# Optimization experiments

Measured on AMD Instinct MI355X. Metric: run time of the kernel, lower is better.

## Reference

```python
import jax, jax.numpy as jnp
import numpy as np

N_NODES = 100000
D_FEAT = 256
BATCH = 16384
K_SAMPLE = 10


def setup_inputs() -> dict:
    key = jax.random.key(0)
    k1, k2, k3, k4 = jax.random.split(key, 4)
    features = jax.random.normal(k1, (N_NODES, D_FEAT), dtype=jnp.float32)
    neigh_idx = jax.random.randint(k2, (BATCH, K_SAMPLE), 0, N_NODES, dtype=jnp.int64)
    nodes = jax.random.randint(k3, (BATCH,), 0, N_NODES, dtype=jnp.int64)
    # models np.random.permutation row shuffle of the embedding matrix
    perm = jax.random.permutation(k4, N_NODES).astype(jnp.int64)
    return {"features": features, "neigh_idx": neigh_idx, "nodes": nodes, "perm": perm}


def reference(features, neigh_idx, nodes, perm):
    # mask.mm(embed): mean over K sampled neighbors' features  -> [B, D]
    to_feats = jnp.mean(features[neigh_idx], axis=1)
    # shuffled embedding matrix = features[perm]; mask.mm(shuf_embed)
    shuf_to_feats = jnp.mean(features[perm[neigh_idx]], axis=1)
    # mask_self.mm(embed): gather own-node row  -> [B, D]
    skip_feats = features[nodes]
    shuf_skip_feats = features[perm[nodes]]
    return (to_feats, shuf_to_feats, skip_feats, shuf_skip_feats)
```

## Files before the change

### kernel.cpp

```cpp
#include <hip/hip_runtime.h>


typedef float f32x4 __attribute__((ext_vector_type(4)));

constexpr int BATCH    = 16384;
constexpr int K_SAMPLE = 10;
constexpr int D_FEAT   = 256;
constexpr int SLICES   = 8;
constexpr int SLICE_D  = D_FEAT / SLICES;
constexpr int CHUNK    = 32;
constexpr int THREADS  = 256;

__global__ __launch_bounds__(THREADS)
void mean_agg_kernel(const float* __restrict__ features,
                     const int*   __restrict__ neigh_idx,
                     const int*   __restrict__ nodes,
                     const int*   __restrict__ perm,
                     float*       __restrict__ out)
{
    const int slice = blockIdx.x & (SLICES - 1);
    const int chunk = blockIdx.x >> 3;

    const int t     = threadIdx.x;
    const int g     = t >> 3;
    const int lane8 = t & 7;

    const int b = chunk * CHUNK + g;
    const int d = slice * SLICE_D + lane8 * 4;

    const int n  = nodes[b];
    const int pn = perm[n];
    const f32x4 o2 = *reinterpret_cast<const f32x4*>(
        &features[(size_t)n  * D_FEAT + d]);
    const f32x4 o3 = *reinterpret_cast<const f32x4*>(
        &features[(size_t)pn * D_FEAT + d]);

    f32x4 acc  = {0.f, 0.f, 0.f, 0.f};
    f32x4 accs = {0.f, 0.f, 0.f, 0.f};

    #pragma unroll
    for (int k = 0; k < K_SAMPLE; ++k) {
        const int idx  = neigh_idx[b * K_SAMPLE + k];
        const int pidx = perm[idx];
        const f32x4 f  = *reinterpret_cast<const f32x4*>(
            &features[(size_t)idx  * D_FEAT + d]);
        const f32x4 fs = *reinterpret_cast<const f32x4*>(
            &features[(size_t)pidx * D_FEAT + d]);
        acc  += f;
        accs += fs;
    }

    const float inv = 1.0f / (float)K_SAMPLE;
    const f32x4 o0 = acc  * inv;
    const f32x4 o1 = accs * inv;

    const size_t row = (size_t)b * D_FEAT + d;
    const size_t sec = (size_t)BATCH * D_FEAT;
    __builtin_nontemporal_store(o0, reinterpret_cast<f32x4*>(&out[row]          ));
    __builtin_nontemporal_store(o1, reinterpret_cast<f32x4*>(&out[row +     sec]));
    __builtin_nontemporal_store(o2, reinterpret_cast<f32x4*>(&out[row + 2 * sec]));
    __builtin_nontemporal_store(o3, reinterpret_cast<f32x4*>(&out[row + 3 * sec]));
}

extern "C" void kernel_launch(void* const* d_in, const int* in_sizes, int n_in,
                              void* d_out, int out_size, void* d_ws, size_t ws_size,
                              hipStream_t stream) {
    const float* features  = (const float*)d_in[0];
    const int*   neigh_idx = (const int*)  d_in[1];
    const int*   nodes     = (const int*)  d_in[2];
    const int*   perm      = (const int*)  d_in[3];
    float*       out       = (float*)d_out;

    const int grid = (BATCH / CHUNK) * SLICES;
    mean_agg_kernel<<<grid, THREADS, 0, stream>>>(features, neigh_idx, nodes, perm, out);
}
```

Baseline: 59.61 us.

## Stage gather indices in LDS and split feature gathers into node-range phases

Loads neighbor indices, node ids and their perm lookups once per block into shared memory instead of redundantly per lane group. Splits the feature gather loop into four phases by node-index range, separated by block barriers, aiming to improve cache locality of the random row reads. The phasing adds branches and barriers that limit how many independent loads are in flight, and the locality benefit depends on blocks progressing in step, which is not enforced across the grid.

```diff
diff --git a/kernel.cpp b/kernel.cpp
--- a/kernel.cpp
+++ b/kernel.cpp
@@ -6,10 +6,13 @@
 constexpr int BATCH    = 16384;
 constexpr int K_SAMPLE = 10;
 constexpr int D_FEAT   = 256;
+constexpr int N_NODES  = 100000;
 constexpr int SLICES   = 8;
 constexpr int SLICE_D  = D_FEAT / SLICES;
 constexpr int CHUNK    = 32;
 constexpr int THREADS  = 256;
+constexpr int PHASES   = 4;
+constexpr int RANGE    = N_NODES / PHASES;
 
 __global__ __launch_bounds__(THREADS)
 void mean_agg_kernel(const float* __restrict__ features,
@@ -28,26 +31,53 @@
     const int b = chunk * CHUNK + g;
     const int d = slice * SLICE_D + lane8 * 4;
 
-    const int n  = nodes[b];
-    const int pn = perm[n];
-    const f32x4 o2 = *reinterpret_cast<const f32x4*>(
-        &features[(size_t)n  * D_FEAT + d]);
-    const f32x4 o3 = *reinterpret_cast<const f32x4*>(
-        &features[(size_t)pn * D_FEAT + d]);
+    __shared__ int s_idx [CHUNK * K_SAMPLE];
+    __shared__ int s_pidx[CHUNK * K_SAMPLE];
+    __shared__ int s_n [CHUNK];
+    __shared__ int s_pn[CHUNK];
+
+    for (int i = t; i < CHUNK * K_SAMPLE; i += THREADS) {
+        const int idx = neigh_idx[chunk * CHUNK * K_SAMPLE + i];
+        s_idx [i] = idx;
+        s_pidx[i] = perm[idx];
+    }
+    if (t < CHUNK) {
+        const int n = nodes[chunk * CHUNK + t];
+        s_n [t] = n;
+        s_pn[t] = perm[n];
+    }
+    __syncthreads();
 
     f32x4 acc  = {0.f, 0.f, 0.f, 0.f};
     f32x4 accs = {0.f, 0.f, 0.f, 0.f};
+    f32x4 o2   = {0.f, 0.f, 0.f, 0.f};
+    f32x4 o3   = {0.f, 0.f, 0.f, 0.f};
 
-    #pragma unroll
-    for (int k = 0; k < K_SAMPLE; ++k) {
-        const int idx  = neigh_idx[b * K_SAMPLE + k];
-        const int pidx = perm[idx];
-        const f32x4 f  = *reinterpret_cast<const f32x4*>(
-            &features[(size_t)idx  * D_FEAT + d]);
-        const f32x4 fs = *reinterpret_cast<const f32x4*>(
-            &features[(size_t)pidx * D_FEAT + d]);
-        acc  += f;
-        accs += fs;
+    for (int p = 0; p < PHASES; ++p) {
+        const int lo = p * RANGE;
+        const int hi = lo + RANGE;
+
+        #pragma unroll
+        for (int k = 0; k < K_SAMPLE; ++k) {
+            const int idx = s_idx[g * K_SAMPLE + k];
+            if (idx >= lo && idx < hi)
+                acc += *reinterpret_cast<const f32x4*>(
+                    &features[(size_t)idx * D_FEAT + d]);
+            const int pidx = s_pidx[g * K_SAMPLE + k];
+            if (pidx >= lo && pidx < hi)
+                accs += *reinterpret_cast<const f32x4*>(
+                    &features[(size_t)pidx * D_FEAT + d]);
+        }
+        const int n = s_n[g];
+        if (n >= lo && n < hi)
+            o2 = *reinterpret_cast<const f32x4*>(
+                &features[(size_t)n * D_FEAT + d]);
+        const int pn = s_pn[g];
+        if (pn >= lo && pn < hi)
+            o3 = *reinterpret_cast<const f32x4*>(
+                &features[(size_t)pn * D_FEAT + d]);
+
+        __syncthreads();
     }
 
     const float inv = 1.0f / (float)K_SAMPLE;
```

Result: slower. 74.26 us (+24.6%).

## Split neighbor gathers into node-range phases to improve cache locality

Applied to the files above, without the earlier changes.

Preloads all neighbor and permuted indices into registers, then gathers feature rows in two phases, each covering half of the node ID range. Alternating block generations start on opposite halves, and a barrier separates the phases so blocks tend to touch the same half of the feature table together, aiming for better L2/MALL hit rates. The cost is a barrier, divergent predicated loads, and less memory-level parallelism per phase. The change is also sensitive to the order in which blocks are scheduled.

```diff
diff --git a/kernel.cpp b/kernel.cpp
--- a/kernel.cpp
+++ b/kernel.cpp
@@ -6,10 +6,13 @@
 constexpr int BATCH    = 16384;
 constexpr int K_SAMPLE = 10;
 constexpr int D_FEAT   = 256;
+constexpr int N_NODES  = 100000;
 constexpr int SLICES   = 8;
 constexpr int SLICE_D  = D_FEAT / SLICES;
 constexpr int CHUNK    = 32;
 constexpr int THREADS  = 256;
+constexpr int PHASES   = 2;
+constexpr int RANGE    = N_NODES / PHASES;
 
 __global__ __launch_bounds__(THREADS)
 void mean_agg_kernel(const float* __restrict__ features,
@@ -20,6 +23,7 @@
 {
     const int slice = blockIdx.x & (SLICES - 1);
     const int chunk = blockIdx.x >> 3;
+    const int gen   = (blockIdx.x >> 11) & 1;
 
     const int t     = threadIdx.x;
     const int g     = t >> 3;
@@ -35,19 +39,31 @@
     const f32x4 o3 = *reinterpret_cast<const f32x4*>(
         &features[(size_t)pn * D_FEAT + d]);
 
+    int idx[K_SAMPLE], pidx[K_SAMPLE];
+    #pragma unroll
+    for (int k = 0; k < K_SAMPLE; ++k) {
+        idx[k]  = neigh_idx[b * K_SAMPLE + k];
+        pidx[k] = perm[idx[k]];
+    }
+
     f32x4 acc  = {0.f, 0.f, 0.f, 0.f};
     f32x4 accs = {0.f, 0.f, 0.f, 0.f};
 
     #pragma unroll
-    for (int k = 0; k < K_SAMPLE; ++k) {
-        const int idx  = neigh_idx[b * K_SAMPLE + k];
-        const int pidx = perm[idx];
-        const f32x4 f  = *reinterpret_cast<const f32x4*>(
-            &features[(size_t)idx  * D_FEAT + d]);
-        const f32x4 fs = *reinterpret_cast<const f32x4*>(
-            &features[(size_t)pidx * D_FEAT + d]);
-        acc  += f;
-        accs += fs;
+    for (int p = 0; p < PHASES; ++p) {
+        const int w  = p ^ gen;
+        const int lo = w * RANGE;
+
+        #pragma unroll
+        for (int k = 0; k < K_SAMPLE; ++k) {
+            if ((unsigned)(idx[k] - lo) < (unsigned)RANGE)
+                acc += *reinterpret_cast<const f32x4*>(
+                    &features[(size_t)idx[k] * D_FEAT + d]);
+            if ((unsigned)(pidx[k] - lo) < (unsigned)RANGE)
+                accs += *reinterpret_cast<const f32x4*>(
+                    &features[(size_t)pidx[k] * D_FEAT + d]);
+        }
+        __syncthreads();
     }
 
     const float inv = 1.0f / (float)K_SAMPLE;
```

After: 71.99 us. +20.8%, slower.
